# Performance work log

Measured on AMD Instinct MI355X. Metric: run time of the kernel, lower is better.

## Reference

```python
import jax, jax.numpy as jnp
import numpy as np

N = 50000
E = 800000
EP = 200000
IN_C = 128
HID = 128


def setup_inputs() -> dict:
    key = jax.random.key(0)
    ks = jax.random.split(key, 10)
    x = jax.random.normal(ks[0], (N, IN_C), dtype=jnp.float32)
    edge_index = jax.random.randint(ks[1], (2, E), 0, N, dtype=jnp.int64)
    pred_edges = jax.random.randint(ks[2], (2, EP), 0, N, dtype=jnp.int64)
    s_in = 1.0 / np.sqrt(IN_C)
    s_h = 1.0 / np.sqrt(HID)
    W1l = jax.random.normal(ks[3], (IN_C, HID), dtype=jnp.float32) * s_in
    W1r = jax.random.normal(ks[4], (IN_C, HID), dtype=jnp.float32) * s_in
    b1 = jnp.zeros((HID,), dtype=jnp.float32)
    W2l = jax.random.normal(ks[5], (HID, HID), dtype=jnp.float32) * s_h
    W2r = jax.random.normal(ks[6], (HID, HID), dtype=jnp.float32) * s_h
    b2 = jnp.zeros((HID,), dtype=jnp.float32)
    return {"x": x, "W1l": W1l, "b1": b1, "W1r": W1r,
            "W2l": W2l, "b2": b2, "W2r": W2r,
            "edge_index": edge_index, "pred_edges": pred_edges}


def _sage_conv(h, Wl, b, Wr, src, dst, n_nodes):
    # PyG SAGEConv (aggr='mean'): out = lin_l(mean_j x_j) + lin_r(x_i)
    msg = h[src]                                              # (E, D) gather
    agg = jax.ops.segment_sum(msg, dst, num_segments=n_nodes)  # (N, D) scatter-add
    deg = jax.ops.segment_sum(jnp.ones((src.shape[0],), h.dtype), dst,
                              num_segments=n_nodes)
    agg = agg / jnp.maximum(deg, 1.0)[:, None]                # mean (0 for isolated)
    return agg @ Wl + b + h @ Wr


def reference(x, W1l, b1, W1r, W2l, b2, W2r, edge_index, pred_edges):
    n_nodes = x.shape[0]
    src, dst = edge_index[0], edge_index[1]
    h = jax.nn.relu(_sage_conv(x, W1l, b1, W1r, src, dst, n_nodes))
    z = _sage_conv(h, W2l, b2, W2r, src, dst, n_nodes)
    ps, pd = pred_edges[0], pred_edges[1]
    return jnp.sum(z[ps] * z[pd], axis=-1)  # (E_pred,) logits
```

## Files before the change

### kernel.cpp

```cpp
#include <hip/hip_runtime.h>

#define D 128

typedef __attribute__((ext_vector_type(8))) short short8;
typedef __attribute__((ext_vector_type(4))) float f32x4;

__device__ inline unsigned int f2bf_bits(float f) {
    unsigned int u = __float_as_uint(f);
    return (u + 0x7FFFu + ((u >> 16) & 1u)) >> 16;
}

__device__ inline float bfhi(unsigned int u) { return __uint_as_float(u << 16); }
__device__ inline float bflo(unsigned int u) { return __uint_as_float(u & 0xffff0000u); }

__global__ __launch_bounds__(256) void prep_kernel(
    const float* __restrict__ x,
    const float* __restrict__ W1l, const float* __restrict__ W1r,
    const float* __restrict__ W2l, const float* __restrict__ W2r,
    unsigned short* __restrict__ xbf, unsigned short* __restrict__ xlo,
    unsigned short* __restrict__ h1, unsigned short* __restrict__ l1,
    unsigned short* __restrict__ h2, unsigned short* __restrict__ l2,
    int n4, int ncast, int* __restrict__ chist, int* __restrict__ csrpad)
{
    const int b = blockIdx.x;
    const int t = threadIdx.x;
    if (b < ncast) {
        int i = b * 256 + t;
        if (i >= n4) return;
        f32x4 v = *(const f32x4*)(x + (size_t)i * 4);
        ushort4 oh, ol;
        {
            unsigned int h; float hf;
            h = f2bf_bits(v.x); hf = __uint_as_float(h << 16);
            oh.x = (unsigned short)h; ol.x = (unsigned short)f2bf_bits(v.x - hf);
            h = f2bf_bits(v.y); hf = __uint_as_float(h << 16);
            oh.y = (unsigned short)h; ol.y = (unsigned short)f2bf_bits(v.y - hf);
            h = f2bf_bits(v.z); hf = __uint_as_float(h << 16);
            oh.z = (unsigned short)h; ol.z = (unsigned short)f2bf_bits(v.z - hf);
            h = f2bf_bits(v.w); hf = __uint_as_float(h << 16);
            oh.w = (unsigned short)h; ol.w = (unsigned short)f2bf_bits(v.w - hf);
        }
        *(ushort4*)(xbf + (size_t)i * 4) = oh;
        *(ushort4*)(xlo + (size_t)i * 4) = ol;
    } else if (b < ncast + 256) {
        int gidx = (b - ncast) * 256 + t;
        int sel = gidx >> 15;
        int idx = gidx & 32767;
        int tt = idx >> 12;
        int ks = (idx >> 9) & 7;
        int lane = (idx >> 3) & 63;
        int j = idx & 7;
        int qq = lane >> 4, r16 = lane & 15;
        int k = ks * 32 + qq * 8 + j;
        int c = tt * 16 + r16;
        const float* Wl = sel ? W2l : W1l;
        const float* Wr = sel ? W2r : W1r;
        float v = (k < 128) ? Wl[k * 128 + c] : Wr[(k - 128) * 128 + c];
        unsigned int h = f2bf_bits(v);
        float hf = __uint_as_float(h << 16);
        unsigned int l = f2bf_bits(v - hf);
        (sel ? h2 : h1)[idx] = (unsigned short)h;
        (sel ? l2 : l1)[idx] = (unsigned short)l;
    } else {
        chist[t] = 0;
        if (t < 16) csrpad[t] = 0;
    }
}

__global__ __launch_bounds__(256) void coarse_count_kernel(const int* __restrict__ dst,
                                                           int* __restrict__ chist, int E) {
    __shared__ int h[256];
    h[threadIdx.x] = 0;
    __syncthreads();
    const int stride = gridDim.x * 256;
    for (int e = blockIdx.x * 256 + threadIdx.x; e < E; e += stride)
        atomicAdd(&h[dst[e] >> 8], 1);
    __syncthreads();
    int v = h[threadIdx.x];
    if (v) atomicAdd(&chist[threadIdx.x], v);
}

__global__ __launch_bounds__(256) void scan256_kernel(const int* __restrict__ chist,
                                                      int* __restrict__ cbase,
                                                      int* __restrict__ gcur) {
    __shared__ int wsum[4];
    const int t = threadIdx.x, lane = t & 63, wv = t >> 6;
    int v = chist[t];
    int s = v;
#pragma unroll
    for (int o = 1; o < 64; o <<= 1) {
        int u = __shfl_up(s, o, 64);
        if (lane >= o) s += u;
    }
    if (lane == 63) wsum[wv] = s;
    __syncthreads();
    int add = 0;
    for (int w = 0; w < wv; ++w) add += wsum[w];
    cbase[t + 1] = s + add;
    if (t == 0) cbase[0] = 0;
    gcur[t] = s + add - v;
}

#define CCHUNK 4096
__global__ __launch_bounds__(256) void coarse_scatter_kernel(
    const int* __restrict__ src, const int* __restrict__ dst,
    int* __restrict__ gcur, unsigned int* __restrict__ centries, int E)
{
    __shared__ int h[256];
    __shared__ int base[256];
    __shared__ unsigned int stage[CCHUNK];
    const int t = threadIdx.x;
    const int e0 = blockIdx.x * CCHUNK;
    h[t] = 0;
    __syncthreads();
#pragma unroll
    for (int i = 0; i < 16; ++i) {
        int e = e0 + i * 256 + t;
        unsigned int u = 0xFFFFFFFFu;
        if (e < E) {
            int d = dst[e];
            int s = src[e];
            int b = d >> 8;
            u = ((unsigned)b << 24) | ((unsigned)s << 8) | (unsigned)(d & 255);
            atomicAdd(&h[b], 1);
        }
        stage[i * 256 + t] = u;
    }
    __syncthreads();
    base[t] = atomicAdd(&gcur[t], h[t]);
    __syncthreads();
    h[t] = 0;
    __syncthreads();
#pragma unroll
    for (int i = 0; i < 16; ++i) {
        unsigned int u = stage[i * 256 + t];
        if (u != 0xFFFFFFFFu) {
            int b = u >> 24;
            int r = atomicAdd(&h[b], 1);
            centries[base[b] + r] = u & 0x00FFFFFFu;
        }
    }
}

#define DCAP 8192
__global__ __launch_bounds__(256) void fine_bucket_kernel(
    const unsigned int* __restrict__ centries,
    const int* __restrict__ cbase,
    int* __restrict__ offo, int* __restrict__ csr, int N, int E)
{
    __shared__ int h[256], ex[256], wsum[4];
    __shared__ int stg[DCAP];
    const int t = threadIdx.x, lane = t & 63, wv = t >> 6;
    const int b = blockIdx.x;
    const int s0 = cbase[b];
    const int cnt = cbase[b + 1] - s0;
    h[t] = 0;
    __syncthreads();
    for (int i = t; i < cnt; i += 256)
        atomicAdd(&h[centries[s0 + i] & 255], 1);
    __syncthreads();
    int v = h[t], s = v;
#pragma unroll
    for (int o = 1; o < 64; o <<= 1) {
        int u = __shfl_up(s, o, 64);
        if (lane >= o) s += u;
    }
    if (lane == 63) wsum[wv] = s;
    __syncthreads();
    int add = 0;
    for (int w = 0; w < wv; ++w) add += wsum[w];
    const int exc = s + add - v;
    ex[t] = exc;
    const int dg = b * 256 + t;
    if (dg < N) offo[dg] = s0 + exc;
    if (b == 0 && t == 0) offo[N] = E;
    h[t] = 0;
    __syncthreads();
    if (cnt <= DCAP) {
        for (int i = t; i < cnt; i += 256) {
            unsigned int u = centries[s0 + i];
            int dl = u & 255;
            int r = atomicAdd(&h[dl], 1);
            stg[ex[dl] + r] = (int)(u >> 8);
        }
        __syncthreads();
        for (int i = t; i < cnt; i += 256)
            csr[s0 + i] = stg[i];
    } else {
        for (int i = t; i < cnt; i += 256) {
            unsigned int u = centries[s0 + i];
            int dl = u & 255;
            int r = atomicAdd(&h[dl], 1);
            csr[s0 + ex[dl] + r] = (int)(u >> 8);
        }
    }
}

__global__ __launch_bounds__(256) void gather_mean_kernel(
    const unsigned short* __restrict__ featbf,
    const int* __restrict__ off,
    const int* __restrict__ csr,
    unsigned short* __restrict__ agg_hi,
    unsigned short* __restrict__ agg_lo,
    int n_nodes)
{
    const int hw = (blockIdx.x * 256 + threadIdx.x) >> 5;
    const int l5 = threadIdx.x & 31;
    if (hw >= n_nodes) return;
    const unsigned short* fb = featbf + (size_t)l5 * 4;
    const int start = off[hw];
    const int end = off[hw + 1];
    f32x4 acc = {0.f, 0.f, 0.f, 0.f};
    for (int e = start; e < end; e += 16) {
        int4 ia = *(const int4*)(csr + e);
        int4 ib = *(const int4*)(csr + e + 4);
        int4 ic = *(const int4*)(csr + e + 8);
        int4 id = *(const int4*)(csr + e + 12);
        uint2 r[16];
        r[0]  = *(const uint2*)(fb + (size_t)ia.x * D);
        r[1]  = *(const uint2*)(fb + (size_t)ia.y * D);
        r[2]  = *(const uint2*)(fb + (size_t)ia.z * D);
        r[3]  = *(const uint2*)(fb + (size_t)ia.w * D);
        r[4]  = *(const uint2*)(fb + (size_t)ib.x * D);
        r[5]  = *(const uint2*)(fb + (size_t)ib.y * D);
        r[6]  = *(const uint2*)(fb + (size_t)ib.z * D);
        r[7]  = *(const uint2*)(fb + (size_t)ib.w * D);
        r[8]  = *(const uint2*)(fb + (size_t)ic.x * D);
        r[9]  = *(const uint2*)(fb + (size_t)ic.y * D);
        r[10] = *(const uint2*)(fb + (size_t)ic.z * D);
        r[11] = *(const uint2*)(fb + (size_t)ic.w * D);
        r[12] = *(const uint2*)(fb + (size_t)id.x * D);
        r[13] = *(const uint2*)(fb + (size_t)id.y * D);
        r[14] = *(const uint2*)(fb + (size_t)id.z * D);
        r[15] = *(const uint2*)(fb + (size_t)id.w * D);
#pragma unroll
        for (int p = 0; p < 16; ++p) {
            uint2 rv = r[p];
            if (e + p >= end) { rv.x = 0u; rv.y = 0u; }
            acc.x += __uint_as_float(rv.x << 16);
            acc.y += __uint_as_float(rv.x & 0xffff0000u);
            acc.z += __uint_as_float(rv.y << 16);
            acc.w += __uint_as_float(rv.y & 0xffff0000u);
        }
    }
    float dinv = 1.0f / (float)max(end - start, 1);
    acc *= dinv;
    const int tile = hw >> 4, r16 = hw & 15;
    const int ks = l5 >> 3, qc = (l5 & 7) >> 1, jb = (l5 & 1) * 4;
    const size_t p = ((size_t)(tile * 4 + ks) * 64 + qc * 16 + r16) * 8 + jb;
    ushort4 oh, ol;
#pragma unroll
    for (int i = 0; i < 4; ++i) {
        float v = acc[i];
        unsigned int h = f2bf_bits(v);
        float hf = __uint_as_float(h << 16);
        ((unsigned short*)&oh)[i] = (unsigned short)h;
        ((unsigned short*)&ol)[i] = (unsigned short)f2bf_bits(v - hf);
    }
    *(ushort4*)(agg_hi + p) = oh;
    *(ushort4*)(agg_lo + p) = ol;
}

__device__ inline void loadb8(const unsigned short* __restrict__ bh,
                              const unsigned short* __restrict__ bl,
                              int ks, short8* BH, short8* BL) {
    const unsigned short* p = bh + (size_t)ks * 512;
    const unsigned short* q = bl + (size_t)ks * 512;
#pragma unroll
    for (int t = 0; t < 8; ++t) {
        BH[t] = *(const short8*)(p + (size_t)t * 4096);
        BL[t] = *(const short8*)(q + (size_t)t * 4096);
    }
}

__device__ inline void mfma24(const short8& AH, const short8& AL,
                              const short8* BH, const short8* BL, f32x4* acc) {
#pragma unroll
    for (int t = 0; t < 8; ++t) {
        acc[t] = __builtin_amdgcn_mfma_f32_16x16x32_bf16(AH, BH[t], acc[t], 0, 0, 0);
        acc[t] = __builtin_amdgcn_mfma_f32_16x16x32_bf16(AL, BH[t], acc[t], 0, 0, 0);
        acc[t] = __builtin_amdgcn_mfma_f32_16x16x32_bf16(AH, BL[t], acc[t], 0, 0, 0);
    }
}

__global__ __launch_bounds__(256, 2) void sage_gemm_kernel(
    const unsigned short* __restrict__ agg_hi,
    const unsigned short* __restrict__ agg_lo,
    const unsigned short* __restrict__ self_hi,
    const unsigned short* __restrict__ self_lo,
    const unsigned short* __restrict__ wpk_hi,
    const unsigned short* __restrict__ wpk_lo,
    const float* __restrict__ bias,
    unsigned short* __restrict__ out_hi,
    unsigned short* __restrict__ out_lo,
    int ntiles, int do_relu)
{
    const int wv = threadIdx.x >> 6;
    const int lane = threadIdx.x & 63;
    const int tile = blockIdx.x * 4 + wv;
    if (tile >= ntiles) return;
    const int q = lane >> 4, r16 = lane & 15;
    const int n0w = tile * 16;

    f32x4 acc8[8];
#pragma unroll
    for (int t = 0; t < 8; ++t) acc8[t] = (f32x4){0.f, 0.f, 0.f, 0.f};

    const unsigned short* aph = agg_hi + (size_t)tile * 2048 + lane * 8;
    const unsigned short* apl = agg_lo + (size_t)tile * 2048 + lane * 8;
    const unsigned short* sph = self_hi + (size_t)(n0w + r16) * D + q * 8;
    const unsigned short* spl = self_lo + (size_t)(n0w + r16) * D + q * 8;
    const unsigned short* bh  = wpk_hi + lane * 8;
    const unsigned short* bl  = wpk_lo + lane * 8;

#define LOADA(ks, AH, AL)                                           \
    if ((ks) < 4) {                                                 \
        AH = *(const short8*)(aph + (ks) * 512);                    \
        AL = *(const short8*)(apl + (ks) * 512);                    \
    } else {                                                        \
        AH = *(const short8*)(sph + ((ks) - 4) * 32);               \
        AL = *(const short8*)(spl + ((ks) - 4) * 32);               \
    }

    short8 BH0[8], BL0[8], BH1[8], BL1[8];
    short8 AH0, AL0, AH1, AL1;

    loadb8(bh, bl, 0, BH0, BL0); LOADA(0, AH0, AL0);
    loadb8(bh, bl, 1, BH1, BL1); LOADA(1, AH1, AL1);
    mfma24(AH0, AL0, BH0, BL0, acc8);
    loadb8(bh, bl, 2, BH0, BL0); LOADA(2, AH0, AL0);
    mfma24(AH1, AL1, BH1, BL1, acc8);
    loadb8(bh, bl, 3, BH1, BL1); LOADA(3, AH1, AL1);
    mfma24(AH0, AL0, BH0, BL0, acc8);
    loadb8(bh, bl, 4, BH0, BL0); LOADA(4, AH0, AL0);
    mfma24(AH1, AL1, BH1, BL1, acc8);
    loadb8(bh, bl, 5, BH1, BL1); LOADA(5, AH1, AL1);
    mfma24(AH0, AL0, BH0, BL0, acc8);
    loadb8(bh, bl, 6, BH0, BL0); LOADA(6, AH0, AL0);
    mfma24(AH1, AL1, BH1, BL1, acc8);
    loadb8(bh, bl, 7, BH1, BL1); LOADA(7, AH1, AL1);
    mfma24(AH0, AL0, BH0, BL0, acc8);
    mfma24(AH1, AL1, BH1, BL1, acc8);
#undef LOADA

#pragma unroll
    for (int t = 0; t < 8; ++t) {
        const float bv = bias[t * 16 + r16];
#pragma unroll
        for (int r = 0; r < 4; ++r) {
            float vv = acc8[t][r] + bv;
            if (do_relu) vv = fmaxf(vv, 0.f);
            const size_t o = (size_t)(n0w + q * 4 + r) * D + t * 16 + r16;
            unsigned int h = f2bf_bits(vv);
            out_hi[o] = (unsigned short)h;
            if (out_lo) {
                float hf = __uint_as_float(h << 16);
                out_lo[o] = (unsigned short)f2bf_bits(vv - hf);
            }
        }
    }
}

__global__ __launch_bounds__(256) void pred_kernel(const unsigned short* __restrict__ zbf,
                                                   const int* __restrict__ ps,
                                                   const int* __restrict__ pd,
                                                   float* __restrict__ out, int EP) {
    int idx = blockIdx.x * blockDim.x + threadIdx.x;
    int e = idx >> 5;
    if (e >= EP) return;
    int l = idx & 31;
    const unsigned short* fb = zbf + (size_t)l * 4;
    uint2 ra = *(const uint2*)(fb + (size_t)ps[e] * D);
    uint2 rb = *(const uint2*)(fb + (size_t)pd[e] * D);
    float p = __uint_as_float(ra.x << 16)         * __uint_as_float(rb.x << 16)
            + __uint_as_float(ra.x & 0xffff0000u) * __uint_as_float(rb.x & 0xffff0000u)
            + __uint_as_float(ra.y << 16)         * __uint_as_float(rb.y << 16)
            + __uint_as_float(ra.y & 0xffff0000u) * __uint_as_float(rb.y & 0xffff0000u);
#pragma unroll
    for (int off = 16; off > 0; off >>= 1) p += __shfl_xor(p, off, 32);
    if (l == 0) out[e] = p;
}

extern "C" void kernel_launch(void* const* d_in, const int* in_sizes, int n_in,
                              void* d_out, int out_size, void* d_ws, size_t ws_size,
                              hipStream_t stream) {
    const float* x   = (const float*)d_in[0];
    const float* W1l = (const float*)d_in[1];
    const float* b1  = (const float*)d_in[2];
    const float* W1r = (const float*)d_in[3];
    const float* W2l = (const float*)d_in[4];
    const float* b2  = (const float*)d_in[5];
    const float* W2r = (const float*)d_in[6];
    const int* edge_index = (const int*)d_in[7];
    const int* pred_edges = (const int*)d_in[8];
    float* out = (float*)d_out;

    const int N  = in_sizes[0] / D;
    const int E  = in_sizes[7] / 2;
    const int EP = in_sizes[8] / 2;

    const int* src = edge_index;
    const int* dst = edge_index + E;
    const int* ps  = pred_edges;
    const int* pd  = pred_edges + EP;

    int* chist   = (int*)d_ws;
    int* cbase   = chist + 256;
    int* gcur    = cbase + 272;
    int* off     = gcur + 256;
    unsigned int* centries = (unsigned int*)(off + 50016);
    int* csr     = (int*)(centries + E);
    unsigned short* w1_hi = (unsigned short*)(csr + E + 16);
    unsigned short* w1_lo = w1_hi + 32768;
    unsigned short* w2_hi = w1_lo + 32768;
    unsigned short* w2_lo = w2_hi + 32768;
    unsigned short* xbf   = w2_lo + 32768;
    unsigned short* xlo   = xbf + (size_t)N * D;
    unsigned short* hbf   = xlo + (size_t)N * D;
    unsigned short* hlo   = hbf + (size_t)N * D;
    unsigned short* zbf   = hlo + (size_t)N * D;
    unsigned short* agg_hi = zbf + (size_t)N * D;
    unsigned short* agg_lo = agg_hi + (size_t)N * D;

    const int n4 = N * D / 4;
    const int ncast = (n4 + 255) / 256;
    const int nblk_gather = (N * 32 + 255) / 256;
    const int ntiles = N / 16;
    const int nblk_gemm = (ntiles + 3) / 4;
    const int nbC = (E + CCHUNK - 1) / CCHUNK;
    const int nbD = (N + 255) / 256;
    const int nblk_pred = (EP * 32 + 255) / 256;

    prep_kernel<<<ncast + 257, 256, 0, stream>>>(x, W1l, W1r, W2l, W2r,
                                                 xbf, xlo, w1_hi, w1_lo, w2_hi, w2_lo,
                                                 n4, ncast, chist, csr + E);

    coarse_count_kernel<<<256, 256, 0, stream>>>(dst, chist, E);
    scan256_kernel<<<1, 256, 0, stream>>>(chist, cbase, gcur);
    coarse_scatter_kernel<<<nbC, 256, 0, stream>>>(src, dst, gcur, centries, E);
    fine_bucket_kernel<<<nbD, 256, 0, stream>>>(centries, cbase, off, csr, N, E);

    gather_mean_kernel<<<nblk_gather, 256, 0, stream>>>(xbf, off, csr, agg_hi, agg_lo, N);
    sage_gemm_kernel<<<nblk_gemm, 256, 0, stream>>>(agg_hi, agg_lo, xbf, xlo,
                                                    w1_hi, w1_lo, b1, hbf, hlo, ntiles, 1);
    gather_mean_kernel<<<nblk_gather, 256, 0, stream>>>(hbf, off, csr, agg_hi, agg_lo, N);
    sage_gemm_kernel<<<nblk_gemm, 256, 0, stream>>>(agg_hi, agg_lo, hbf, hlo,
                                                    w2_hi, w2_lo, b2, zbf, (unsigned short*)nullptr,
                                                    ntiles, 0);
    pred_kernel<<<nblk_pred, 256, 0, stream>>>(zbf, ps, pd, out, EP);
}
```

Measured before the change: 276.0 us.

## Fuse neighbor mean-gather into the SAGE GEMM kernel, dropping the agg buffers

Merges the gather-mean kernel into the MFMA GEMM kernel. Each wave now gathers neighbor features for its own 16-node tile straight into registers, with 4 lanes per node each reading 64 bytes per neighbor, then splits the mean into hi/lo bf16 A fragments. This removes the write and read of the agg_hi/agg_lo intermediates and two kernel launches per layer. In exchange the gather now runs with far fewer threads per node (4 lanes instead of 32), and a larger register footprint may cut occupancy and latency hiding for the irregular loads.

```diff
diff --git a/kernel.cpp b/kernel.cpp
--- a/kernel.cpp
+++ b/kernel.cpp
@@ -196,71 +196,6 @@
     }
 }
 
-__global__ __launch_bounds__(256) void gather_mean_kernel(
-    const unsigned short* __restrict__ featbf,
-    const int* __restrict__ off,
-    const int* __restrict__ csr,
-    unsigned short* __restrict__ agg_hi,
-    unsigned short* __restrict__ agg_lo,
-    int n_nodes)
-{
-    const int hw = (blockIdx.x * 256 + threadIdx.x) >> 5;
-    const int l5 = threadIdx.x & 31;
-    if (hw >= n_nodes) return;
-    const unsigned short* fb = featbf + (size_t)l5 * 4;
-    const int start = off[hw];
-    const int end = off[hw + 1];
-    f32x4 acc = {0.f, 0.f, 0.f, 0.f};
-    for (int e = start; e < end; e += 16) {
-        int4 ia = *(const int4*)(csr + e);
-        int4 ib = *(const int4*)(csr + e + 4);
-        int4 ic = *(const int4*)(csr + e + 8);
-        int4 id = *(const int4*)(csr + e + 12);
-        uint2 r[16];
-        r[0]  = *(const uint2*)(fb + (size_t)ia.x * D);
-        r[1]  = *(const uint2*)(fb + (size_t)ia.y * D);
-        r[2]  = *(const uint2*)(fb + (size_t)ia.z * D);
-        r[3]  = *(const uint2*)(fb + (size_t)ia.w * D);
-        r[4]  = *(const uint2*)(fb + (size_t)ib.x * D);
-        r[5]  = *(const uint2*)(fb + (size_t)ib.y * D);
-        r[6]  = *(const uint2*)(fb + (size_t)ib.z * D);
-        r[7]  = *(const uint2*)(fb + (size_t)ib.w * D);
-        r[8]  = *(const uint2*)(fb + (size_t)ic.x * D);
-        r[9]  = *(const uint2*)(fb + (size_t)ic.y * D);
-        r[10] = *(const uint2*)(fb + (size_t)ic.z * D);
-        r[11] = *(const uint2*)(fb + (size_t)ic.w * D);
-        r[12] = *(const uint2*)(fb + (size_t)id.x * D);
-        r[13] = *(const uint2*)(fb + (size_t)id.y * D);
-        r[14] = *(const uint2*)(fb + (size_t)id.z * D);
-        r[15] = *(const uint2*)(fb + (size_t)id.w * D);
-#pragma unroll
-        for (int p = 0; p < 16; ++p) {
-            uint2 rv = r[p];
-            if (e + p >= end) { rv.x = 0u; rv.y = 0u; }
-            acc.x += __uint_as_float(rv.x << 16);
-            acc.y += __uint_as_float(rv.x & 0xffff0000u);
-            acc.z += __uint_as_float(rv.y << 16);
-            acc.w += __uint_as_float(rv.y & 0xffff0000u);
-        }
-    }
-    float dinv = 1.0f / (float)max(end - start, 1);
-    acc *= dinv;
-    const int tile = hw >> 4, r16 = hw & 15;
-    const int ks = l5 >> 3, qc = (l5 & 7) >> 1, jb = (l5 & 1) * 4;
-    const size_t p = ((size_t)(tile * 4 + ks) * 64 + qc * 16 + r16) * 8 + jb;
-    ushort4 oh, ol;
-#pragma unroll
-    for (int i = 0; i < 4; ++i) {
-        float v = acc[i];
-        unsigned int h = f2bf_bits(v);
-        float hf = __uint_as_float(h << 16);
-        ((unsigned short*)&oh)[i] = (unsigned short)h;
-        ((unsigned short*)&ol)[i] = (unsigned short)f2bf_bits(v - hf);
-    }
-    *(ushort4*)(agg_hi + p) = oh;
-    *(ushort4*)(agg_lo + p) = ol;
-}
-
 __device__ inline void loadb8(const unsigned short* __restrict__ bh,
                               const unsigned short* __restrict__ bl,
                               int ks, short8* BH, short8* BL) {
@@ -283,9 +218,10 @@
     }
 }
 
-__global__ __launch_bounds__(256, 2) void sage_gemm_kernel(
-    const unsigned short* __restrict__ agg_hi,
-    const unsigned short* __restrict__ agg_lo,
+__global__ __launch_bounds__(256, 2) void fused_sage_kernel(
+    const unsigned short* __restrict__ featbf,
+    const int* __restrict__ off,
+    const int* __restrict__ csr,
     const unsigned short* __restrict__ self_hi,
     const unsigned short* __restrict__ self_lo,
     const unsigned short* __restrict__ wpk_hi,
@@ -301,47 +237,106 @@
     if (tile >= ntiles) return;
     const int q = lane >> 4, r16 = lane & 15;
     const int n0w = tile * 16;
+    const int node = n0w + r16;
+
+    const unsigned short* bh = wpk_hi + lane * 8;
+    const unsigned short* bl = wpk_lo + lane * 8;
+
+    short8 BH0[8], BL0[8], BH1[8], BL1[8];
+    loadb8(bh, bl, 0, BH0, BL0);
+
+    const int start = off[node];
+    const int end   = off[node + 1];
+    const unsigned short* fb = featbf + q * 8;
+    float ga[4][8];
+#pragma unroll
+    for (int k = 0; k < 4; ++k)
+#pragma unroll
+        for (int c = 0; c < 8; ++c) ga[k][c] = 0.f;
+
+#define ACCUM(rv, k)                                                     \
+    { ga[k][0] += bfhi(rv.x); ga[k][1] += bflo(rv.x);                    \
+      ga[k][2] += bfhi(rv.y); ga[k][3] += bflo(rv.y);                    \
+      ga[k][4] += bfhi(rv.z); ga[k][5] += bflo(rv.z);                    \
+      ga[k][6] += bfhi(rv.w); ga[k][7] += bflo(rv.w); }
+
+    const uint4 zero4 = {0u, 0u, 0u, 0u};
+    for (int e = start; e < end; e += 4) {
+        int4 ix = *(const int4*)(csr + e);
+        const unsigned short* p0 = fb + (size_t)ix.x * D;
+        const unsigned short* p1 = fb + (size_t)ix.y * D;
+        const unsigned short* p2 = fb + (size_t)ix.z * D;
+        const unsigned short* p3 = fb + (size_t)ix.w * D;
+        uint4 r00 = *(const uint4*)(p0);
+        uint4 r01 = *(const uint4*)(p0 + 32);
+        uint4 r02 = *(const uint4*)(p0 + 64);
+        uint4 r03 = *(const uint4*)(p0 + 96);
+        uint4 r10 = *(const uint4*)(p1);
+        uint4 r11 = *(const uint4*)(p1 + 32);
+        uint4 r12 = *(const uint4*)(p1 + 64);
+        uint4 r13 = *(const uint4*)(p1 + 96);
+        uint4 r20 = *(const uint4*)(p2);
+        uint4 r21 = *(const uint4*)(p2 + 32);
+        uint4 r22 = *(const uint4*)(p2 + 64);
+        uint4 r23 = *(const uint4*)(p2 + 96);
+        uint4 r30 = *(const uint4*)(p3);
+        uint4 r31 = *(const uint4*)(p3 + 32);
+        uint4 r32 = *(const uint4*)(p3 + 64);
+        uint4 r33 = *(const uint4*)(p3 + 96);
+        if (e + 1 >= end) { r10 = zero4; r11 = zero4; r12 = zero4; r13 = zero4; }
+        if (e + 2 >= end) { r20 = zero4; r21 = zero4; r22 = zero4; r23 = zero4; }
+        if (e + 3 >= end) { r30 = zero4; r31 = zero4; r32 = zero4; r33 = zero4; }
+        ACCUM(r00, 0) ACCUM(r01, 1) ACCUM(r02, 2) ACCUM(r03, 3)
+        ACCUM(r10, 0) ACCUM(r11, 1) ACCUM(r12, 2) ACCUM(r13, 3)
+        ACCUM(r20, 0) ACCUM(r21, 1) ACCUM(r22, 2) ACCUM(r23, 3)
+        ACCUM(r30, 0) ACCUM(r31, 1) ACCUM(r32, 2) ACCUM(r33, 3)
+    }
+#undef ACCUM
+
+    const float dinv = 1.0f / (float)max(end - start, 1);
+    short8 AH[4], AL[4];
+#pragma unroll
+    for (int k = 0; k < 4; ++k) {
+#pragma unroll
+        for (int c = 0; c < 8; ++c) {
+            float v = ga[k][c] * dinv;
+            unsigned int hbits = f2bf_bits(v);
+            AH[k][c] = (short)hbits;
+            AL[k][c] = (short)f2bf_bits(v - __uint_as_float(hbits << 16));
+        }
+    }
 
     f32x4 acc8[8];
 #pragma unroll
     for (int t = 0; t < 8; ++t) acc8[t] = (f32x4){0.f, 0.f, 0.f, 0.f};
 
-    const unsigned short* aph = agg_hi + (size_t)tile * 2048 + lane * 8;
-    const unsigned short* apl = agg_lo + (size_t)tile * 2048 + lane * 8;
-    const unsigned short* sph = self_hi + (size_t)(n0w + r16) * D + q * 8;
-    const unsigned short* spl = self_lo + (size_t)(n0w + r16) * D + q * 8;
-    const unsigned short* bh  = wpk_hi + lane * 8;
-    const unsigned short* bl  = wpk_lo + lane * 8;
-
-#define LOADA(ks, AH, AL)                                           \
-    if ((ks) < 4) {                                                 \
-        AH = *(const short8*)(aph + (ks) * 512);                    \
-        AL = *(const short8*)(apl + (ks) * 512);                    \
-    } else {                                                        \
-        AH = *(const short8*)(sph + ((ks) - 4) * 32);               \
-        AL = *(const short8*)(spl + ((ks) - 4) * 32);               \
-    }
-
-    short8 BH0[8], BL0[8], BH1[8], BL1[8];
-    short8 AH0, AL0, AH1, AL1;
-
-    loadb8(bh, bl, 0, BH0, BL0); LOADA(0, AH0, AL0);
-    loadb8(bh, bl, 1, BH1, BL1); LOADA(1, AH1, AL1);
-    mfma24(AH0, AL0, BH0, BL0, acc8);
-    loadb8(bh, bl, 2, BH0, BL0); LOADA(2, AH0, AL0);
-    mfma24(AH1, AL1, BH1, BL1, acc8);
-    loadb8(bh, bl, 3, BH1, BL1); LOADA(3, AH1, AL1);
-    mfma24(AH0, AL0, BH0, BL0, acc8);
-    loadb8(bh, bl, 4, BH0, BL0); LOADA(4, AH0, AL0);
-    mfma24(AH1, AL1, BH1, BL1, acc8);
-    loadb8(bh, bl, 5, BH1, BL1); LOADA(5, AH1, AL1);
-    mfma24(AH0, AL0, BH0, BL0, acc8);
-    loadb8(bh, bl, 6, BH0, BL0); LOADA(6, AH0, AL0);
-    mfma24(AH1, AL1, BH1, BL1, acc8);
-    loadb8(bh, bl, 7, BH1, BL1); LOADA(7, AH1, AL1);
-    mfma24(AH0, AL0, BH0, BL0, acc8);
-    mfma24(AH1, AL1, BH1, BL1, acc8);
-#undef LOADA
+    const unsigned short* sph = self_hi + (size_t)node * D + q * 8;
+    const unsigned short* spl = self_lo + (size_t)node * D + q * 8;
+
+    short8 SH0, SL0, SH1, SL1;
+    loadb8(bh, bl, 1, BH1, BL1);
+    SH0 = *(const short8*)(sph);
+    SL0 = *(const short8*)(spl);
+    mfma24(AH[0], AL[0], BH0, BL0, acc8);
+    loadb8(bh, bl, 2, BH0, BL0);
+    SH1 = *(const short8*)(sph + 32);
+    SL1 = *(const short8*)(spl + 32);
+    mfma24(AH[1], AL[1], BH1, BL1, acc8);
+    loadb8(bh, bl, 3, BH1, BL1);
+    mfma24(AH[2], AL[2], BH0, BL0, acc8);
+    loadb8(bh, bl, 4, BH0, BL0);
+    mfma24(AH[3], AL[3], BH1, BL1, acc8);
+    loadb8(bh, bl, 5, BH1, BL1);
+    mfma24(SH0, SL0, BH0, BL0, acc8);
+    loadb8(bh, bl, 6, BH0, BL0);
+    SH0 = *(const short8*)(sph + 64);
+    SL0 = *(const short8*)(spl + 64);
+    mfma24(SH1, SL1, BH1, BL1, acc8);
+    loadb8(bh, bl, 7, BH1, BL1);
+    SH1 = *(const short8*)(sph + 96);
+    SL1 = *(const short8*)(spl + 96);
+    mfma24(SH0, SL0, BH0, BL0, acc8);
+    mfma24(SH1, SL1, BH1, BL1, acc8);
 
 #pragma unroll
     for (int t = 0; t < 8; ++t) {
@@ -419,12 +414,9 @@
     unsigned short* hbf   = xlo + (size_t)N * D;
     unsigned short* hlo   = hbf + (size_t)N * D;
     unsigned short* zbf   = hlo + (size_t)N * D;
-    unsigned short* agg_hi = zbf + (size_t)N * D;
-    unsigned short* agg_lo = agg_hi + (size_t)N * D;
 
     const int n4 = N * D / 4;
     const int ncast = (n4 + 255) / 256;
-    const int nblk_gather = (N * 32 + 255) / 256;
     const int ntiles = N / 16;
     const int nblk_gemm = (ntiles + 3) / 4;
     const int nbC = (E + CCHUNK - 1) / CCHUNK;
@@ -440,12 +432,10 @@
     coarse_scatter_kernel<<<nbC, 256, 0, stream>>>(src, dst, gcur, centries, E);
     fine_bucket_kernel<<<nbD, 256, 0, stream>>>(centries, cbase, off, csr, N, E);
 
-    gather_mean_kernel<<<nblk_gather, 256, 0, stream>>>(xbf, off, csr, agg_hi, agg_lo, N);
-    sage_gemm_kernel<<<nblk_gemm, 256, 0, stream>>>(agg_hi, agg_lo, xbf, xlo,
-                                                    w1_hi, w1_lo, b1, hbf, hlo, ntiles, 1);
-    gather_mean_kernel<<<nblk_gather, 256, 0, stream>>>(hbf, off, csr, agg_hi, agg_lo, N);
-    sage_gemm_kernel<<<nblk_gemm, 256, 0, stream>>>(agg_hi, agg_lo, hbf, hlo,
-                                                    w2_hi, w2_lo, b2, zbf, (unsigned short*)nullptr,
-                                                    ntiles, 0);
+    fused_sage_kernel<<<nblk_gemm, 256, 0, stream>>>(xbf, off, csr, xbf, xlo,
+                                                     w1_hi, w1_lo, b1, hbf, hlo, ntiles, 1);
+    fused_sage_kernel<<<nblk_gemm, 256, 0, stream>>>(hbf, off, csr, hbf, hlo,
+                                                     w2_hi, w2_lo, b2, zbf,
+                                                     (unsigned short*)nullptr, ntiles, 0);
     pred_kernel<<<nblk_pred, 256, 0, stream>>>(zbf, ps, pd, out, EP);
 }
```

Result: slower. 282.3 us (+2.3%).
